# Optimization experiments

Measured on AMD Instinct MI355X. Metric: run time of the kernel, lower is better.

## Reference

```python
import jax, jax.numpy as jnp
import numpy as np

B, T = 64, 64
H = 256
CLIP = 0.2


def _conv(x, W, b, s):
    y = jax.lax.conv_general_dilated(x, W, (s, s), 'VALID',
                                     dimension_numbers=('NHWC', 'HWIO', 'NHWC'))
    return jax.nn.leaky_relu(y + b, negative_slope=0.2)


def _lstm(x, Wk, Wr, b):
    # keras LSTM, gate order i,f,g,o; x: (B,T,256) -> (B,T,256)
    h0 = jnp.zeros((x.shape[0], H), x.dtype)

    def step(carry, xt):
        h, c = carry
        z = xt @ Wk + h @ Wr + b
        i, f, g, o = jnp.split(z, 4, axis=-1)
        c = jax.nn.sigmoid(f) * c + jax.nn.sigmoid(i) * jnp.tanh(g)
        h = jax.nn.sigmoid(o) * jnp.tanh(c)
        return (h, c), h

    _, hs = jax.lax.scan(step, (h0, h0), jnp.swapaxes(x, 0, 1))
    return jnp.swapaxes(hs, 0, 1)


def setup_inputs():
    key = jax.random.key(0)
    ks = jax.random.split(key, 24)
    s = 0.05
    x = jax.random.normal(ks[0], (B, T, 13, 8, 8), jnp.float32)
    a_taken = jax.random.randint(ks[1], (B, T), 0, 36)
    mask = jax.random.randint(ks[2], (B, T, 4096), 0, 2).astype(jnp.int32)
    # taken actions must be legal (mask=1), as in real rollouts
    bi = jnp.repeat(jnp.arange(B), T)
    ti = jnp.tile(jnp.arange(T), B)
    mask = mask.at[bi, ti, a_taken.reshape(-1)].set(1)
    lg_prob_old = -jnp.abs(jax.random.normal(ks[3], (B, T), jnp.float32)) - 1.0
    GAE = jax.random.normal(ks[4], (B, T), jnp.float32)
    old_v_pred = jax.random.normal(ks[5], (B, T), jnp.float32)
    returns = jax.random.normal(ks[6], (B, T), jnp.float32)
    return {
        'x': x, 'mask': mask, 'lg_prob_old': lg_prob_old, 'a_taken': a_taken,
        'GAE': GAE, 'old_v_pred': old_v_pred, 'returns': returns,
        'W1': jax.random.normal(ks[7], (2, 2, 8, 16), jnp.float32) * s,
        'b1': jnp.zeros((16,), jnp.float32),
        'W2': jax.random.normal(ks[8], (2, 2, 16, 32), jnp.float32) * s,
        'b2': jnp.zeros((32,), jnp.float32),
        'W3': jax.random.normal(ks[9], (2, 2, 32, 64), jnp.float32) * s,
        'b3': jnp.zeros((64,), jnp.float32),
        'W4': jax.random.normal(ks[10], (1, 1, 64, 128), jnp.float32) * s,
        'b4': jnp.zeros((128,), jnp.float32),
        'lstm_k': jax.random.normal(ks[11], (256, 1024), jnp.float32) * s,
        'lstm_r': jax.random.normal(ks[12], (256, 1024), jnp.float32) * s,
        'lstm_b': jnp.zeros((1024,), jnp.float32),
        'pir_W': jax.random.normal(ks[13], (256, 36), jnp.float32) * s,
        'pir_b': jnp.zeros((36,), jnp.float32),
        'pim_W': jax.random.normal(ks[14], (256, 4096), jnp.float32) * s,
        'pim_b': jnp.zeros((4096,), jnp.float32),
        'v_W': jax.random.normal(ks[15], (256, 1), jnp.float32) * s,
        'v_b': jnp.zeros((1,), jnp.float32),
    }


def reference(x, mask, lg_prob_old, a_taken, GAE, old_v_pred, returns,
              W1, b1, W2, b2, W3, b3, W4, b4,
              lstm_k, lstm_r, lstm_b, pir_W, pir_b, pim_W, pim_b, v_W, v_b):
    Bn, Tn = x.shape[0], x.shape[1]
    h = x.reshape(Bn * Tn, 13, 8, 8)  # NHWC: H=13, W=8, C=8
    h = _conv(h, W1, b1, 2)  # (BT,6,4,16)
    h = _conv(h, W2, b2, 1)  # (BT,5,3,32)
    h = _conv(h, W3, b3, 2)  # (BT,2,1,64)
    h = _conv(h, W4, b4, 1)  # (BT,2,1,128)
    # keras Flatten(data_format='channels_first') permutes dim1 to last then flattens
    h = jnp.transpose(h, (0, 2, 3, 1)).reshape(Bn, Tn, -1)  # (B,T,256)
    lstm = _lstm(h, lstm_k, lstm_r, lstm_b).reshape(-1, H)  # (BT,256)

    pir = jax.nn.softmax(lstm @ pir_W + pir_b, axis=-1)  # (BT,36)
    maskf = mask.reshape(-1, 4096).astype(jnp.float32)
    pim = jax.nn.softmax(lstm @ pim_W + pim_b, axis=-1) * maskf
    scale = jnp.sum(pim, axis=1, keepdims=True)
    pim = pim / jnp.where(scale > 0, scale, jnp.ones_like(scale))  # (BT,4096)
    vpred = lstm @ v_W + v_b  # (BT,1)

    lg_old = lg_prob_old.reshape(-1)
    a = a_taken.reshape(-1)
    gae = GAE.reshape(-1)
    ovp = old_v_pred.reshape(-1)
    ret = returns.reshape(-1)
    gae = (gae - jnp.mean(gae)) / (jnp.std(gae) + 1e-8)

    t = jnp.arange(a.shape[0])
    p = jnp.where(t % 2 == 0, pir[t, a], pim[t, a])  # alternating heads
    lg_new = jnp.log(p)
    rt = jnp.exp(lg_new - lg_old)
    pg1 = -gae * rt
    pg2 = -gae * jnp.clip(rt, 1.0 - CLIP, 1.0 + CLIP)
    pg_loss = jnp.mean(jnp.maximum(pg1, pg2))

    # faithful to original TF: (BT,1) vpred broadcast against (BT,) -> (BT,BT)
    vpredclipped = ovp + jnp.clip(vpred - ovp, -CLIP, CLIP)
    vf1 = jnp.square(vpred - ret)
    vf2 = jnp.square(vpredclipped - ret)
    vf_loss = 0.5 * jnp.mean(jnp.maximum(vf1, vf2))

    pim_e = pim + (1.0 - maskf)
    entropy = -jnp.sum(pir * jnp.log(pir)) - jnp.sum(pim_e * jnp.log(pim_e))
    loss = pg_loss - entropy + vf_loss
    return (loss, pg_loss, entropy, vf_loss)
```

## Files before the change

kernel.cpp:

```cpp
#include <hip/hip_runtime.h>

typedef unsigned short u16;
typedef unsigned int   u32;

#define BT   4096
#define TSEQ 64
#define NB   64

typedef __attribute__((ext_vector_type(8))) short  short8;
typedef __attribute__((ext_vector_type(4))) float  f32x4;
typedef __attribute__((ext_vector_type(2))) _Float16 h2;

__device__ __forceinline__ float bf(u16 v) {
    u32 u = ((u32)v) << 16;
    return __builtin_bit_cast(float, u);
}
__device__ __forceinline__ u16 f2b(float f) {
    u32 u = __builtin_bit_cast(u32, f);
    return (u16)((u + 0x7fffu + ((u >> 16) & 1u)) >> 16);
}
__device__ __forceinline__ float lrelu(float x) { return x > 0.f ? x : 0.2f * x; }
__device__ __forceinline__ h2 i2h(int v) { return __builtin_bit_cast(h2, v); }
__device__ __forceinline__ float dot2(int hbits, int wbits, float acc) {
#if __has_builtin(__builtin_amdgcn_fdot2)
    return __builtin_amdgcn_fdot2(i2h(hbits), i2h(wbits), acc, false);
#else
    h2 a = i2h(hbits), b = i2h(wbits);
    return acc + (float)a.x * (float)b.x + (float)a.y * (float)b.y;
#endif
}
__device__ __forceinline__ float fsigm(float x) { return 1.f / (1.f + __expf(-x)); }
__device__ __forceinline__ float ftanh(float x) { return 1.f - 2.f / (__expf(2.f * x) + 1.f); }
__device__ __forceinline__ float ldf(const void* p, int i, int f32) {
    return f32 ? ((const float*)p)[i] : bf(((const u16*)p)[i]);
}
__device__ __forceinline__ u16 ldb(const void* p, int i, int f32) {
    return f32 ? f2b(((const float*)p)[i]) : ((const u16*)p)[i];
}

struct PrepPtrs {
    const void *x, *W1, *b1, *W2, *b2, *W3, *b3, *W4, *b4;
    const void *Wr, *Wk, *Wpim, *Wpir, *Wv;
    const u16* probe;
    u16 *featbf, *PF, *PBk, *PBpim, *PBpir;
    float* scal; int* flag;
};

#define PACK_BLKS 776
#define CONV_BLKS 2048

__global__ __launch_bounds__(256) void prep_kernel(PrepPtrs P)
{
    const int bid = blockIdx.x, tid = threadIdx.x;
    const int lane = tid & 63;
    u16 pv = P.probe[2 * lane];
    int e = (pv >> 7) & 0xFF;
    unsigned long long m = __ballot(pv == 0 || (e >= 100 && e <= 130));
    const int f32 = (__popcll(m) < 48) ? 1 : 0;

    if (bid == 0 && tid < 32) { P.scal[tid] = 0.f; if (tid == 0) *P.flag = f32; }

    if (bid < PACK_BLKS) {
        u16 t8[8];
        if (bid < 128) {
            int gid = bid * 256 + tid;
            int col = gid & 1023, oct = gid >> 10;
#pragma unroll
            for (int j = 0; j < 8; j++) {
                float f = ldf(P.Wr, (oct * 8 + j) * 1024 + col, f32);
                _Float16 h = (_Float16)f;
                t8[j] = __builtin_bit_cast(unsigned short, h);
            }
            *(int4*)&P.PF[((size_t)oct * 1024 + col) * 8] = *(int4*)t8;
        } else if (bid < 256) {
            int gid = (bid - 128) * 256 + tid;
            int col = gid & 1023, oct = gid >> 10;
#pragma unroll
            for (int j = 0; j < 8; j++) t8[j] = ldb(P.Wk, (oct * 8 + j) * 1024 + col, f32);
            *(int4*)&P.PBk[((((size_t)(oct >> 2) << 10) + col) * 4 + (oct & 3)) * 8] = *(int4*)t8;
        } else if (bid < 768) {
            int gid = (bid - 256) * 256 + tid;
            int col = gid & 4095, oct = gid >> 12;
#pragma unroll
            for (int j = 0; j < 8; j++) t8[j] = ldb(P.Wpim, (size_t)(oct * 8 + j) * 4096 + col, f32);
            *(int4*)&P.PBpim[((((size_t)(oct >> 2) << 12) + col) * 4 + (oct & 3)) * 8] = *(int4*)t8;
        } else {
            int gid = (bid - 768) * 256 + tid;
            int col = gid & 63, oct = gid >> 6;
#pragma unroll
            for (int j = 0; j < 8; j++) {
                int k = oct * 8 + j;
                u16 v = 0;
                if (col < 36)       v = ldb(P.Wpir, k * 36 + col, f32);
                else if (col == 36) v = ldb(P.Wv, k, f32);
                t8[j] = v;
            }
            *(int4*)&P.PBpir[(((size_t)(oct >> 2) * 64 + col) * 4 + (oct & 3)) * 8] = *(int4*)t8;
        }
        return;
    }

    __shared__ __align__(16) u16 wl[19184];
    __shared__ float xs[2][832];
    __shared__ float c1[2][384];
    __shared__ float c2[2][480];
    __shared__ float c3[2][128];
    const int pair = bid - PACK_BLKS;
    const int sub = tid >> 7, stid = tid & 127;
    const int bt = pair * 2 + sub;

    {
        const void* sp[8] = {P.W1, P.b1, P.W2, P.b2, P.W3, P.b3, P.W4, P.b4};
        const int   sn[8] = {512, 16, 2048, 32, 8192, 64, 8192, 128};
        int o = 0;
        for (int s = 0; s < 8; s++) {
            for (int i = tid; i < sn[s]; i += 256) wl[o + i] = ldb(sp[s], i, f32);
            o += sn[s];
        }
    }
    for (int i = stid; i < 832; i += 128) xs[sub][i] = ldf(P.x, bt * 832 + i, f32);
    __syncthreads();

    for (int idx = stid; idx < 96; idx += 128) {
        int pos = idx >> 2, g = idx & 3;
        int oh = pos >> 2, ow = pos & 3;
        float a0 = bf(wl[512 + g * 4]), a1 = bf(wl[513 + g * 4]),
              a2 = bf(wl[514 + g * 4]), a3 = bf(wl[515 + g * 4]);
        for (int kh = 0; kh < 2; kh++)
            for (int kw = 0; kw < 2; kw++)
#pragma unroll
                for (int ic = 0; ic < 8; ic++) {
                    float xv = xs[sub][(2 * oh + kh) * 64 + (2 * ow + kw) * 8 + ic];
                    ushort4 w = *(const ushort4*)&wl[((kh * 2 + kw) * 8 + ic) * 16 + g * 4];
                    a0 += xv * bf(w.x); a1 += xv * bf(w.y);
                    a2 += xv * bf(w.z); a3 += xv * bf(w.w);
                }
        c1[sub][pos * 16 + g * 4]     = lrelu(a0);
        c1[sub][pos * 16 + g * 4 + 1] = lrelu(a1);
        c1[sub][pos * 16 + g * 4 + 2] = lrelu(a2);
        c1[sub][pos * 16 + g * 4 + 3] = lrelu(a3);
    }
    __syncthreads();

    for (int idx = stid; idx < 120; idx += 128) {
        int pos = idx >> 3, g = idx & 7;
        int oh = pos / 3, ow = pos % 3;
        float a0 = bf(wl[2576 + g * 4]), a1 = bf(wl[2577 + g * 4]),
              a2 = bf(wl[2578 + g * 4]), a3 = bf(wl[2579 + g * 4]);
        for (int kh = 0; kh < 2; kh++)
            for (int kw = 0; kw < 2; kw++)
#pragma unroll
                for (int ic = 0; ic < 16; ic++) {
                    float xv = c1[sub][((oh + kh) * 4 + (ow + kw)) * 16 + ic];
                    ushort4 w = *(const ushort4*)&wl[528 + ((kh * 2 + kw) * 16 + ic) * 32 + g * 4];
                    a0 += xv * bf(w.x); a1 += xv * bf(w.y);
                    a2 += xv * bf(w.z); a3 += xv * bf(w.w);
                }
        c2[sub][pos * 32 + g * 4]     = lrelu(a0);
        c2[sub][pos * 32 + g * 4 + 1] = lrelu(a1);
        c2[sub][pos * 32 + g * 4 + 2] = lrelu(a2);
        c2[sub][pos * 32 + g * 4 + 3] = lrelu(a3);
    }
    __syncthreads();

    for (int idx = stid; idx < 32; idx += 128) {
        int oh = idx >> 4, g = idx & 15;
        float a0 = bf(wl[10800 + g * 4]), a1 = bf(wl[10801 + g * 4]),
              a2 = bf(wl[10802 + g * 4]), a3 = bf(wl[10803 + g * 4]);
        for (int kh = 0; kh < 2; kh++)
            for (int kw = 0; kw < 2; kw++)
#pragma unroll
                for (int ic = 0; ic < 32; ic++) {
                    float xv = c2[sub][((2 * oh + kh) * 3 + kw) * 32 + ic];
                    ushort4 w = *(const ushort4*)&wl[2608 + ((kh * 2 + kw) * 32 + ic) * 64 + g * 4];
                    a0 += xv * bf(w.x); a1 += xv * bf(w.y);
                    a2 += xv * bf(w.z); a3 += xv * bf(w.w);
                }
        c3[sub][oh * 64 + g * 4]     = lrelu(a0);
        c3[sub][oh * 64 + g * 4 + 1] = lrelu(a1);
        c3[sub][oh * 64 + g * 4 + 2] = lrelu(a2);
        c3[sub][oh * 64 + g * 4 + 3] = lrelu(a3);
    }
    __syncthreads();

    for (int idx = stid; idx < 64; idx += 128) {
        int oh = idx >> 5, g = idx & 31;
        float a0 = bf(wl[19056 + g * 4]), a1 = bf(wl[19057 + g * 4]),
              a2 = bf(wl[19058 + g * 4]), a3 = bf(wl[19059 + g * 4]);
#pragma unroll
        for (int ic = 0; ic < 64; ic++) {
            float xv = c3[sub][oh * 64 + ic];
            ushort4 w = *(const ushort4*)&wl[10864 + ic * 128 + g * 4];
            a0 += xv * bf(w.x); a1 += xv * bf(w.y);
            a2 += xv * bf(w.z); a3 += xv * bf(w.w);
        }
        P.featbf[bt * 256 + (g * 4 + 0) * 2 + oh] = f2b(lrelu(a0));
        P.featbf[bt * 256 + (g * 4 + 1) * 2 + oh] = f2b(lrelu(a1));
        P.featbf[bt * 256 + (g * 4 + 2) * 2 + oh] = f2b(lrelu(a2));
        P.featbf[bt * 256 + (g * 4 + 3) * 2 + oh] = f2b(lrelu(a3));
    }
}

__global__ __launch_bounds__(256) void gemm_zx(
    const u16* __restrict__ Abf, const u16* __restrict__ PB,
    const void* __restrict__ bias, const int* __restrict__ flag,
    float* __restrict__ out)
{
    __shared__ __align__(16) u16 As[16 * 264];
    const int mb = blockIdx.y, nb = blockIdx.x, tid = threadIdx.x;
    const int f32 = *flag;
    const int m0 = mb * 16;
    {
        int row = tid >> 4, part = tid & 15;
        const f32x4* src = (const f32x4*)&Abf[(size_t)(m0 + row) * 256 + part * 16];
        f32x4 v0 = src[0], v1 = src[1];
        *(f32x4*)&As[row * 264 + part * 16] = v0;
        *(f32x4*)&As[row * 264 + part * 16 + 8] = v1;
    }
    __syncthreads();
    const int wv = tid >> 6, lane = tid & 63;
    const int colw = lane & 15, q = lane >> 4;
    const int n = nb * 64 + wv * 16 + colw;
    f32x4 acc = {0.f, 0.f, 0.f, 0.f};
#pragma unroll
    for (int kt = 0; kt < 8; kt++) {
        short8 a = *(const short8*)&As[colw * 264 + kt * 32 + q * 8];
        short8 b = *(const short8*)&PB[((((size_t)kt << 10) + n) * 4 + q) * 8];
        acc = __builtin_amdgcn_mfma_f32_16x16x32_bf16(a, b, acc, 0, 0, 0);
    }
    const float bj = ldf(bias, n, f32);
#pragma unroll
    for (int r = 0; r < 4; r++) {
        int row = q * 4 + r;
        out[(size_t)(m0 + row) * 1024 + n] = acc[r] + bj;
    }
}

#define NPRE 18
#define NLDS 7
#define NSTR (32 - NPRE - NLDS)
__global__ __launch_bounds__(1024)
__attribute__((amdgpu_waves_per_eu(4, 4)))
void lstm_kernel(
    const float* __restrict__ zx, const u16* __restrict__ PF,
    u16* __restrict__ hseqbf)
{
    __shared__ float zp[1024];
    __shared__ __align__(16) u16 h16[256];
    __shared__ u16 hist[TSEQ * 256];
    __shared__ __align__(16) int4 wlds[NLDS * 1024];
    const int b = blockIdx.x, tid = threadIdx.x;
    float c = 0.f;
    const int4* Pw = (const int4*)PF;

    int4 wr[NPRE];
#pragma unroll
    for (int j = 0; j < NPRE; j++) wr[j] = Pw[j * 1024 + tid];
#pragma unroll
    for (int j = 0; j < NLDS; j++) wlds[j * 1024 + tid] = Pw[(NPRE + j) * 1024 + tid];
    if (tid < 256) h16[tid] = 0;
    __syncthreads();

    for (int t = 0; t < TSEQ; t++) {
        int4 ws[NSTR];
#pragma unroll
        for (int j = 0; j < NSTR; j++) ws[j] = Pw[(NPRE + NLDS + j) * 1024 + tid];
        float zxv = zx[(size_t)(b * TSEQ + t) * 1024 + tid];

        float a0 = 0.f, a1 = 0.f, a2 = 0.f, a3 = 0.f;
#pragma unroll
        for (int j = 0; j < NPRE; j++) {
            int4 hv = *(const int4*)&h16[j * 8];
            a0 = dot2(hv.x, wr[j].x, a0);
            a1 = dot2(hv.y, wr[j].y, a1);
            a2 = dot2(hv.z, wr[j].z, a2);
            a3 = dot2(hv.w, wr[j].w, a3);
        }
#pragma unroll
        for (int j = 0; j < NLDS; j++) {
            int4 hv = *(const int4*)&h16[(NPRE + j) * 8];
            int4 w = wlds[j * 1024 + tid];
            a0 = dot2(hv.x, w.x, a0);
            a1 = dot2(hv.y, w.y, a1);
            a2 = dot2(hv.z, w.z, a2);
            a3 = dot2(hv.w, w.w, a3);
        }
#pragma unroll
        for (int j = 0; j < NSTR; j++) {
            int4 hv = *(const int4*)&h16[(NPRE + NLDS + j) * 8];
            a0 = dot2(hv.x, ws[j].x, a0);
            a1 = dot2(hv.y, ws[j].y, a1);
            a2 = dot2(hv.z, ws[j].z, a2);
            a3 = dot2(hv.w, ws[j].w, a3);
        }
        zp[tid] = ((a0 + a1) + (a2 + a3)) + zxv;
        __syncthreads();
        if (tid < 256) {
            float ai = zp[tid], af = zp[256 + tid], ag = zp[512 + tid], ao = zp[768 + tid];
            float ig = fsigm(ai), fg = fsigm(af), og = fsigm(ao);
            float gg = ftanh(ag);
            c = fg * c + ig * gg;
            float h = og * ftanh(c);
            h16[tid] = __builtin_bit_cast(unsigned short, (_Float16)h);
            hist[t * 256 + tid] = f2b(h);
        }
        __syncthreads();
    }
    for (int i = tid; i < TSEQ * 256; i += 1024)
        hseqbf[(size_t)b * (TSEQ * 256) + i] = hist[i];
}

__global__ __launch_bounds__(256) void pir_kernel(
    const u16* __restrict__ Abf, const u16* __restrict__ PB,
    const void* __restrict__ pir_b, const void* __restrict__ v_b,
    const int* __restrict__ flag, const int* __restrict__ a_taken,
    float* __restrict__ entpir, float* __restrict__ ppira, float* __restrict__ vpred)
{
    __shared__ __align__(16) u16 As[64 * 264];
    const int tid = threadIdx.x;
    const int wv = tid >> 6, lane = tid & 63;
    const int colw = lane & 15, q = lane >> 4;
    const int f32 = *flag;
    const int m0 = blockIdx.x * 64;

    for (int idx = tid; idx < 1024; idx += 256) {
        int row = idx >> 4, part = idx & 15;
        const f32x4* src = (const f32x4*)&Abf[(size_t)(m0 + row) * 256 + part * 16];
        f32x4 v0 = src[0], v1 = src[1];
        *(f32x4*)&As[row * 264 + part * 16] = v0;
        *(f32x4*)&As[row * 264 + part * 16 + 8] = v1;
    }
    __syncthreads();
    f32x4 acc[4];
#pragma unroll
    for (int nt = 0; nt < 4; nt++) acc[nt] = (f32x4){0.f, 0.f, 0.f, 0.f};
#pragma unroll
    for (int kt = 0; kt < 8; kt++) {
        short8 a = *(const short8*)&As[(wv * 16 + colw) * 264 + kt * 32 + q * 8];
#pragma unroll
        for (int nt = 0; nt < 4; nt++) {
            short8 b = *(const short8*)&PB[((((size_t)kt * 64) + nt * 16 + colw) * 4 + q) * 8];
            acc[nt] = __builtin_amdgcn_mfma_f32_16x16x32_bf16(a, b, acc[nt], 0, 0, 0);
        }
    }
    float* zq = (float*)&As[wv * 4224];
#pragma unroll
    for (int nt = 0; nt < 4; nt++) {
        int col = nt * 16 + colw;
        float bj = (col < 36) ? ldf(pir_b, col, f32)
                              : (col == 36 ? ldf(v_b, 0, f32) : 0.f);
#pragma unroll
        for (int r = 0; r < 4; r++)
            zq[(q * 4 + r) * 65 + col] = acc[nt][r] + bj;
    }
    if (lane < 16) {
        int R = m0 + wv * 16 + lane;
        const float* zrow = &zq[lane * 65];
        float Z = 0.f, U = 0.f;
        for (int cc = 0; cc < 36; cc++) {
            float z = zrow[cc];
            float ev = __expf(z);
            Z += ev; U += ev * z;
        }
        entpir[R] = logf(Z) - U / Z;
        ppira[R]  = __expf(zrow[a_taken[R]]) / Z;
        vpred[R]  = zrow[36];
    }
}

__global__ __launch_bounds__(256) void pim_kernel(
    const u16* __restrict__ Abf, const u16* __restrict__ PB,
    const void* __restrict__ pim_b, const int* __restrict__ flag,
    const int* __restrict__ mask, const int* __restrict__ a_taken,
    float* __restrict__ partS, float* __restrict__ partU, float* __restrict__ za)
{
    __shared__ __align__(16) u16 As[32 * 264];
    __shared__ float redS[4][32], redU[4][32];
    const int nb = blockIdx.x, mb = blockIdx.y, tid = threadIdx.x;
    const int wv = tid >> 6, lane = tid & 63;
    const int colw = lane & 15, q = lane >> 4;
    const int f32 = *flag;
    const int m0 = mb * 32;

    for (int idx = tid; idx < 512; idx += 256) {
        int row = idx >> 4, part = idx & 15;
        const f32x4* src = (const f32x4*)&Abf[(size_t)(m0 + row) * 256 + part * 16];
        f32x4 v0 = src[0], v1 = src[1];
        *(f32x4*)&As[row * 264 + part * 16] = v0;
        *(f32x4*)&As[row * 264 + part * 16 + 8] = v1;
    }
    __syncthreads();
    const int n = nb * 64 + wv * 16 + colw;
    f32x4 acc0 = {0.f, 0.f, 0.f, 0.f}, acc1 = {0.f, 0.f, 0.f, 0.f};
#pragma unroll
    for (int kt = 0; kt < 8; kt++) {
        short8 b = *(const short8*)&PB[((((size_t)kt << 12) + n) * 4 + q) * 8];
        short8 a0 = *(const short8*)&As[colw * 264 + kt * 32 + q * 8];
        short8 a1 = *(const short8*)&As[(16 + colw) * 264 + kt * 32 + q * 8];
        acc0 = __builtin_amdgcn_mfma_f32_16x16x32_bf16(a0, b, acc0, 0, 0, 0);
        acc1 = __builtin_amdgcn_mfma_f32_16x16x32_bf16(a1, b, acc1, 0, 0, 0);
    }
    const float bj = ldf(pim_b, n, f32);
#pragma unroll
    for (int half = 0; half < 2; half++) {
        const f32x4& acc = half ? acc1 : acc0;
        float sv[4], uv[4];
#pragma unroll
        for (int r = 0; r < 4; r++) {
            int row = m0 + half * 16 + q * 4 + r;
            float z = acc[r] + bj;
            int mm = mask[(size_t)row * 4096 + n];
            float ev = __expf(z);
            sv[r] = mm ? ev : 0.f;
            uv[r] = mm ? ev * z : 0.f;
            if (n == a_taken[row]) za[row] = z;
        }
#pragma unroll
        for (int r = 0; r < 4; r++) {
            for (int off = 1; off < 16; off <<= 1) {
                sv[r] += __shfl_xor(sv[r], off, 16);
                uv[r] += __shfl_xor(uv[r], off, 16);
            }
            if (colw == 0) {
                redS[wv][half * 16 + q * 4 + r] = sv[r];
                redU[wv][half * 16 + q * 4 + r] = uv[r];
            }
        }
    }
    __syncthreads();
    if (tid < 32) {
        float S = redS[0][tid] + redS[1][tid] + redS[2][tid] + redS[3][tid];
        float U = redU[0][tid] + redU[1][tid] + redU[2][tid] + redU[3][tid];
        partS[(size_t)(m0 + tid) * 64 + nb] = S;
        partU[(size_t)(m0 + tid) * 64 + nb] = U;
    }
}

#define TAIL_BLOCKS (16 + 256)
__global__ __launch_bounds__(256) void tail_kernel(
    const float* __restrict__ partS, const float* __restrict__ partU,
    const float* __restrict__ za,
    const float* __restrict__ entpir, const float* __restrict__ ppira,
    const float* __restrict__ vpred,
    const void* __restrict__ lgold, const void* __restrict__ gae,
    const void* __restrict__ ovp, const void* __restrict__ ret,
    float* __restrict__ scal, const int* __restrict__ flag,
    void* __restrict__ out)
{
    const int bid = blockIdx.x, tid = threadIdx.x;
    const int f32 = *flag;
    __shared__ float sh[8];
    __shared__ float mst[2];
    if (bid < 16) {
        const int r = bid * 256 + tid;
        float S = 0.f, U = 0.f;
#pragma unroll
        for (int t2 = 0; t2 < 64; t2++) {
            S += partS[(size_t)r * 64 + t2];
            U += partU[(size_t)r * 64 + t2];
        }
        float entpim = logf(S) - U / S;
        float ppima = __expf(za[r]) / S;
        float s = 0.f, s2 = 0.f;
        if (f32) {
            const float* gp = (const float*)gae;
            for (int i = tid; i < BT; i += 256) { float v = gp[i]; s += v; s2 += v * v; }
        } else {
            const u16* gp = (const u16*)gae;
            for (int i = tid; i < BT; i += 256) { float v = bf(gp[i]); s += v; s2 += v * v; }
        }
        for (int off = 32; off; off >>= 1) {
            s += __shfl_down(s, off, 64); s2 += __shfl_down(s2, off, 64);
        }
        if ((tid & 63) == 0) { sh[tid >> 6] = s; sh[4 + (tid >> 6)] = s2; }
        __syncthreads();
        if (tid == 0) {
            float Sa = sh[0] + sh[1] + sh[2] + sh[3];
            float S2a = sh[4] + sh[5] + sh[6] + sh[7];
            float mean = Sa / (float)BT;
            float var = S2a / (float)BT - mean * mean;
            mst[0] = mean; mst[1] = sqrtf(fmaxf(var, 0.f));
        }
        __syncthreads();
        float mean = mst[0], sd = mst[1];
        float p = (r & 1) ? ppima : ppira[r];
        float ln = logf(p);
        float rt = __expf(ln - ldf(lgold, r, f32));
        float g = (ldf(gae, r, f32) - mean) / (sd + 1e-8f);
        float rtc = fminf(fmaxf(rt, 0.8f), 1.2f);
        float pg = fmaxf(-g * rt, -g * rtc);
        float e12 = entpir[r] + entpim;
        for (int off = 32; off; off >>= 1) {
            pg += __shfl_down(pg, off, 64);
            e12 += __shfl_down(e12, off, 64);
        }
        if ((tid & 63) == 0) {
            atomicAdd(&scal[2], pg);
            atomicAdd(&scal[3], e12);
        }
    } else {
        const int i0 = (bid - 16) * 16;
        float s = 0.f;
        if (f32) {
            const float* rp = (const float*)ret;
            const float* op = (const float*)ovp;
            for (int rr = 0; rr < 16; rr++) {
                float vp = vpred[i0 + rr];
                for (int j = tid; j < BT; j += 256) {
                    float r2 = rp[j], o = op[j];
                    float d = fminf(fmaxf(vp - o, -0.2f), 0.2f);
                    float v1 = vp - r2;    v1 *= v1;
                    float v2 = o + d - r2; v2 *= v2;
                    s += fmaxf(v1, v2);
                }
            }
        } else {
            const u16* rp = (const u16*)ret;
            const u16* op = (const u16*)ovp;
            for (int rr = 0; rr < 16; rr++) {
                float vp = vpred[i0 + rr];
                for (int j = tid; j < BT; j += 256) {
                    float r2 = bf(rp[j]), o = bf(op[j]);
                    float d = fminf(fmaxf(vp - o, -0.2f), 0.2f);
                    float v1 = vp - r2;    v1 *= v1;
                    float v2 = o + d - r2; v2 *= v2;
                    s += fmaxf(v1, v2);
                }
            }
        }
        for (int off = 32; off; off >>= 1) s += __shfl_down(s, off, 64);
        if ((tid & 63) == 0) sh[tid >> 6] = s;
        __syncthreads();
        if (tid == 0) atomicAdd(&scal[5], sh[0] + sh[1] + sh[2] + sh[3]);
    }
    __threadfence();
    __syncthreads();
    if (tid == 0) {
        unsigned old = atomicAdd((unsigned int*)&scal[8], 1u);
        if (old == TAIL_BLOCKS - 1) {
            __threadfence();
            float pgs = atomicAdd(&scal[2], 0.f);
            float ents = atomicAdd(&scal[3], 0.f);
            float vfs = atomicAdd(&scal[5], 0.f);
            float pg = pgs / (float)BT;
            float vf = 0.5f * vfs / ((float)BT * (float)BT);
            float loss = pg - ents + vf;
            if (f32) {
                float* o = (float*)out;
                o[0] = loss; o[1] = pg; o[2] = ents; o[3] = vf;
            } else {
                u16* o = (u16*)out;
                o[0] = f2b(loss); o[1] = f2b(pg); o[2] = f2b(ents); o[3] = f2b(vf);
            }
        }
    }
}

extern "C" void kernel_launch(void* const* d_in, const int* in_sizes, int n_in,
                              void* d_out, int out_size, void* d_ws, size_t ws_size,
                              hipStream_t stream)
{
    const int* mask = (const int*)d_in[1];
    const int* a_tk = (const int*)d_in[3];

    float* p = (float*)d_ws;
    u16*   featbf = (u16*)p;            p += 524288;
    float* zx     = p;                  p += 4194304;
    u16*   hseqbf = (u16*)p;            p += 524288;
    u16*   PF     = (u16*)p;            p += 131072;
    u16*   PBk    = (u16*)p;            p += 131072;
    u16*   PBpim  = (u16*)p;            p += 524288;
    u16*   PBpir  = (u16*)p;            p += 8192;
    float* scal   = p;                  p += 32;
    int*   flag   = (int*)p;            p += 4;
    float* partS  = p;                  p += 262144;
    float* partU  = p;                  p += 262144;
    float* za     = p;                  p += 4096;
    float* entpir = p;                  p += 4096;
    float* ppira  = p;                  p += 4096;
    float* vpred  = p;                  p += 4096;

    PrepPtrs P;
    P.x = d_in[0];
    P.W1 = d_in[7];  P.b1 = d_in[8];
    P.W2 = d_in[9];  P.b2 = d_in[10];
    P.W3 = d_in[11]; P.b3 = d_in[12];
    P.W4 = d_in[13]; P.b4 = d_in[14];
    P.Wk = d_in[15]; P.Wr = d_in[16];
    P.Wpir = d_in[18]; P.Wpim = d_in[20]; P.Wv = d_in[22];
    P.probe = (const u16*)d_in[15];
    P.featbf = featbf; P.PF = PF; P.PBk = PBk; P.PBpim = PBpim; P.PBpir = PBpir;
    P.scal = scal; P.flag = flag;

    prep_kernel<<<PACK_BLKS + CONV_BLKS, 256, 0, stream>>>(P);
    gemm_zx<<<dim3(16, 256), 256, 0, stream>>>(featbf, PBk, d_in[17], flag, zx);
    lstm_kernel<<<NB, 1024, 0, stream>>>(zx, PF, hseqbf);
    pir_kernel<<<64, 256, 0, stream>>>(hseqbf, PBpir, d_in[19], d_in[23], flag,
                                       a_tk, entpir, ppira, vpred);
    pim_kernel<<<dim3(64, 128), 256, 0, stream>>>(hseqbf, PBpim, d_in[21], flag,
                                                  mask, a_tk, partS, partU, za);
    tail_kernel<<<TAIL_BLOCKS, 256, 0, stream>>>(
        partS, partU, za, entpir, ppira, vpred,
        d_in[2], d_in[4], d_in[5], d_in[6], scal, flag, (void*)d_out);
}
```

Before: 488.8 us.

## Store LSTM recurrent weights as fp8 e5m2 and merge head kernels

```diff
diff --git a/kernel.cpp b/kernel.cpp
--- a/kernel.cpp
+++ b/kernel.cpp
@@ -2,6 +2,7 @@
 
 typedef unsigned short u16;
 typedef unsigned int   u32;
+typedef unsigned char  u8;
 
 #define BT   4096
 #define TSEQ 64
@@ -29,6 +30,20 @@
     return acc + (float)a.x * (float)b.x + (float)a.y * (float)b.y;
 #endif
 }
+__device__ __forceinline__ int e5lo(int w) {
+#if __has_builtin(__builtin_amdgcn_perm)
+    return (int)__builtin_amdgcn_perm(0u, (u32)w, 0x010C000Cu);
+#else
+    return ((w & 0xFF) << 8) | ((w & 0xFF00) << 16);
+#endif
+}
+__device__ __forceinline__ int e5hi(int w) {
+#if __has_builtin(__builtin_amdgcn_perm)
+    return (int)__builtin_amdgcn_perm(0u, (u32)w, 0x030C020Cu);
+#else
+    return (((w >> 16) & 0xFF) << 8) | (w & 0xFF000000);
+#endif
+}
 __device__ __forceinline__ float fsigm(float x) { return 1.f / (1.f + __expf(-x)); }
 __device__ __forceinline__ float ftanh(float x) { return 1.f - 2.f / (__expf(2.f * x) + 1.f); }
 __device__ __forceinline__ float ldf(const void* p, int i, int f32) {
@@ -42,7 +57,8 @@
     const void *x, *W1, *b1, *W2, *b2, *W3, *b3, *W4, *b4;
     const void *Wr, *Wk, *Wpim, *Wpir, *Wv;
     const u16* probe;
-    u16 *featbf, *PF, *PBk, *PBpim, *PBpir;
+    u16 *featbf, *PBk, *PBpim, *PBpir;
+    u8* PF8;
     float* scal; int* flag;
 };
 
@@ -61,32 +77,35 @@
     if (bid == 0 && tid < 32) { P.scal[tid] = 0.f; if (tid == 0) *P.flag = f32; }
 
     if (bid < PACK_BLKS) {
-        u16 t8[8];
         if (bid < 128) {
             int gid = bid * 256 + tid;
             int col = gid & 1023, oct = gid >> 10;
+            u8 t8[8];
 #pragma unroll
             for (int j = 0; j < 8; j++) {
                 float f = ldf(P.Wr, (oct * 8 + j) * 1024 + col, f32);
-                _Float16 h = (_Float16)f;
-                t8[j] = __builtin_bit_cast(unsigned short, h);
-            }
-            *(int4*)&P.PF[((size_t)oct * 1024 + col) * 8] = *(int4*)t8;
+                u16 hb = __builtin_bit_cast(unsigned short, (_Float16)f);
+                t8[j] = (u8)((hb + 0x7Fu + ((hb >> 8) & 1u)) >> 8);
+            }
+            *(int2*)&P.PF8[((size_t)oct * 1024 + col) * 8] = *(int2*)t8;
         } else if (bid < 256) {
             int gid = (bid - 128) * 256 + tid;
             int col = gid & 1023, oct = gid >> 10;
+            u16 t8[8];
 #pragma unroll
             for (int j = 0; j < 8; j++) t8[j] = ldb(P.Wk, (oct * 8 + j) * 1024 + col, f32);
             *(int4*)&P.PBk[((((size_t)(oct >> 2) << 10) + col) * 4 + (oct & 3)) * 8] = *(int4*)t8;
         } else if (bid < 768) {
             int gid = (bid - 256) * 256 + tid;
             int col = gid & 4095, oct = gid >> 12;
+            u16 t8[8];
 #pragma unroll
             for (int j = 0; j < 8; j++) t8[j] = ldb(P.Wpim, (size_t)(oct * 8 + j) * 4096 + col, f32);
             *(int4*)&P.PBpim[((((size_t)(oct >> 2) << 12) + col) * 4 + (oct & 3)) * 8] = *(int4*)t8;
         } else {
             int gid = (bid - 768) * 256 + tid;
             int col = gid & 63, oct = gid >> 6;
+            u16 t8[8];
 #pragma unroll
             for (int j = 0; j < 8; j++) {
                 int k = oct * 8 + j;
@@ -236,62 +255,50 @@
     }
 }
 
-#define NPRE 18
-#define NLDS 7
-#define NSTR (32 - NPRE - NLDS)
+#define NLDS8 8
+#define NSTR8 (32 - NLDS8)
 __global__ __launch_bounds__(1024)
 __attribute__((amdgpu_waves_per_eu(4, 4)))
 void lstm_kernel(
-    const float* __restrict__ zx, const u16* __restrict__ PF,
+    const float* __restrict__ zx, const u8* __restrict__ PF8,
     u16* __restrict__ hseqbf)
 {
     __shared__ float zp[1024];
     __shared__ __align__(16) u16 h16[256];
     __shared__ u16 hist[TSEQ * 256];
-    __shared__ __align__(16) int4 wlds[NLDS * 1024];
+    __shared__ __align__(8) int2 wlds[NLDS8 * 1024];
     const int b = blockIdx.x, tid = threadIdx.x;
     float c = 0.f;
-    const int4* Pw = (const int4*)PF;
-
-    int4 wr[NPRE];
-#pragma unroll
-    for (int j = 0; j < NPRE; j++) wr[j] = Pw[j * 1024 + tid];
-#pragma unroll
-    for (int j = 0; j < NLDS; j++) wlds[j * 1024 + tid] = Pw[(NPRE + j) * 1024 + tid];
+    const int2* Pw = (const int2*)PF8;
+
+#pragma unroll
+    for (int j = 0; j < NLDS8; j++) wlds[j * 1024 + tid] = Pw[j * 1024 + tid];
     if (tid < 256) h16[tid] = 0;
     __syncthreads();
 
     for (int t = 0; t < TSEQ; t++) {
-        int4 ws[NSTR];
-#pragma unroll
-        for (int j = 0; j < NSTR; j++) ws[j] = Pw[(NPRE + NLDS + j) * 1024 + tid];
+        int2 ws[NSTR8];
+#pragma unroll
+        for (int j = 0; j < NSTR8; j++) ws[j] = Pw[(NLDS8 + j) * 1024 + tid];
         float zxv = zx[(size_t)(b * TSEQ + t) * 1024 + tid];
 
         float a0 = 0.f, a1 = 0.f, a2 = 0.f, a3 = 0.f;
 #pragma unroll
-        for (int j = 0; j < NPRE; j++) {
+        for (int j = 0; j < NLDS8; j++) {
             int4 hv = *(const int4*)&h16[j * 8];
-            a0 = dot2(hv.x, wr[j].x, a0);
-            a1 = dot2(hv.y, wr[j].y, a1);
-            a2 = dot2(hv.z, wr[j].z, a2);
-            a3 = dot2(hv.w, wr[j].w, a3);
-        }
-#pragma unroll
-        for (int j = 0; j < NLDS; j++) {
-            int4 hv = *(const int4*)&h16[(NPRE + j) * 8];
-            int4 w = wlds[j * 1024 + tid];
-            a0 = dot2(hv.x, w.x, a0);
-            a1 = dot2(hv.y, w.y, a1);
-            a2 = dot2(hv.z, w.z, a2);
-            a3 = dot2(hv.w, w.w, a3);
-        }
-#pragma unroll
-        for (int j = 0; j < NSTR; j++) {
-            int4 hv = *(const int4*)&h16[(NPRE + NLDS + j) * 8];
-            a0 = dot2(hv.x, ws[j].x, a0);
-            a1 = dot2(hv.y, ws[j].y, a1);
-            a2 = dot2(hv.z, ws[j].z, a2);
-            a3 = dot2(hv.w, ws[j].w, a3);
+            int2 w = wlds[j * 1024 + tid];
+            a0 = dot2(hv.x, e5lo(w.x), a0);
+            a1 = dot2(hv.y, e5hi(w.x), a1);
+            a2 = dot2(hv.z, e5lo(w.y), a2);
+            a3 = dot2(hv.w, e5hi(w.y), a3);
+        }
+#pragma unroll
+        for (int j = 0; j < NSTR8; j++) {
+            int4 hv = *(const int4*)&h16[(NLDS8 + j) * 8];
+            a0 = dot2(hv.x, e5lo(ws[j].x), a0);
+            a1 = dot2(hv.y, e5hi(ws[j].x), a1);
+            a2 = dot2(hv.z, e5lo(ws[j].y), a2);
+            a3 = dot2(hv.w, e5hi(ws[j].y), a3);
         }
         zp[tid] = ((a0 + a1) + (a2 + a3)) + zxv;
         __syncthreads();
@@ -310,78 +317,71 @@
         hseqbf[(size_t)b * (TSEQ * 256) + i] = hist[i];
 }
 
-__global__ __launch_bounds__(256) void pir_kernel(
-    const u16* __restrict__ Abf, const u16* __restrict__ PB,
-    const void* __restrict__ pir_b, const void* __restrict__ v_b,
-    const int* __restrict__ flag, const int* __restrict__ a_taken,
-    float* __restrict__ entpir, float* __restrict__ ppira, float* __restrict__ vpred)
+__global__ __launch_bounds__(256) void heads_kernel(
+    const u16* __restrict__ Abf,
+    const u16* __restrict__ PBpim, const u16* __restrict__ PBpir,
+    const void* __restrict__ pim_b, const void* __restrict__ pir_b,
+    const void* __restrict__ v_b, const int* __restrict__ flag,
+    const int* __restrict__ mask, const int* __restrict__ a_taken,
+    float* __restrict__ entpir, float* __restrict__ ppira, float* __restrict__ vpred,
+    float* __restrict__ partS, float* __restrict__ partU, float* __restrict__ za)
 {
     __shared__ __align__(16) u16 As[64 * 264];
+    __shared__ float redS[4][32], redU[4][32];
     const int tid = threadIdx.x;
     const int wv = tid >> 6, lane = tid & 63;
     const int colw = lane & 15, q = lane >> 4;
     const int f32 = *flag;
-    const int m0 = blockIdx.x * 64;
-
-    for (int idx = tid; idx < 1024; idx += 256) {
-        int row = idx >> 4, part = idx & 15;
-        const f32x4* src = (const f32x4*)&Abf[(size_t)(m0 + row) * 256 + part * 16];
-        f32x4 v0 = src[0], v1 = src[1];
-        *(f32x4*)&As[row * 264 + part * 16] = v0;
-        *(f32x4*)&As[row * 264 + part * 16 + 8] = v1;
-    }
-    __syncthreads();
-    f32x4 acc[4];
-#pragma unroll
-    for (int nt = 0; nt < 4; nt++) acc[nt] = (f32x4){0.f, 0.f, 0.f, 0.f};
-#pragma unroll
-    for (int kt = 0; kt < 8; kt++) {
-        short8 a = *(const short8*)&As[(wv * 16 + colw) * 264 + kt * 32 + q * 8];
+
+    if (blockIdx.y == 128) {
+        const int m0 = blockIdx.x * 64;
+        for (int idx = tid; idx < 1024; idx += 256) {
+            int row = idx >> 4, part = idx & 15;
+            const f32x4* src = (const f32x4*)&Abf[(size_t)(m0 + row) * 256 + part * 16];
+            f32x4 v0 = src[0], v1 = src[1];
+            *(f32x4*)&As[row * 264 + part * 16] = v0;
+            *(f32x4*)&As[row * 264 + part * 16 + 8] = v1;
+        }
+        __syncthreads();
+        f32x4 acc[4];
+#pragma unroll
+        for (int nt = 0; nt < 4; nt++) acc[nt] = (f32x4){0.f, 0.f, 0.f, 0.f};
+#pragma unroll
+        for (int kt = 0; kt < 8; kt++) {
+            short8 a = *(const short8*)&As[(wv * 16 + colw) * 264 + kt * 32 + q * 8];
+#pragma unroll
+            for (int nt = 0; nt < 4; nt++) {
+                short8 b = *(const short8*)&PBpir[((((size_t)kt * 64) + nt * 16 + colw) * 4 + q) * 8];
+                acc[nt] = __builtin_amdgcn_mfma_f32_16x16x32_bf16(a, b, acc[nt], 0, 0, 0);
+            }
+        }
+        float* zq = (float*)&As[wv * 4224];
 #pragma unroll
         for (int nt = 0; nt < 4; nt++) {
-            short8 b = *(const short8*)&PB[((((size_t)kt * 64) + nt * 16 + colw) * 4 + q) * 8];
-            acc[nt] = __builtin_amdgcn_mfma_f32_16x16x32_bf16(a, b, acc[nt], 0, 0, 0);
-        }
-    }
-    float* zq = (float*)&As[wv * 4224];
-#pragma unroll
-    for (int nt = 0; nt < 4; nt++) {
-        int col = nt * 16 + colw;
-        float bj = (col < 36) ? ldf(pir_b, col, f32)
-                              : (col == 36 ? ldf(v_b, 0, f32) : 0.f);
-#pragma unroll
-        for (int r = 0; r < 4; r++)
-            zq[(q * 4 + r) * 65 + col] = acc[nt][r] + bj;
-    }
-    if (lane < 16) {
-        int R = m0 + wv * 16 + lane;
-        const float* zrow = &zq[lane * 65];
-        float Z = 0.f, U = 0.f;
-        for (int cc = 0; cc < 36; cc++) {
-            float z = zrow[cc];
-            float ev = __expf(z);
-            Z += ev; U += ev * z;
-        }
-        entpir[R] = logf(Z) - U / Z;
-        ppira[R]  = __expf(zrow[a_taken[R]]) / Z;
-        vpred[R]  = zrow[36];
-    }
-}
-
-__global__ __launch_bounds__(256) void pim_kernel(
-    const u16* __restrict__ Abf, const u16* __restrict__ PB,
-    const void* __restrict__ pim_b, const int* __restrict__ flag,
-    const int* __restrict__ mask, const int* __restrict__ a_taken,
-    float* __restrict__ partS, float* __restrict__ partU, float* __restrict__ za)
-{
-    __shared__ __align__(16) u16 As[32 * 264];
-    __shared__ float redS[4][32], redU[4][32];
-    const int nb = blockIdx.x, mb = blockIdx.y, tid = threadIdx.x;
-    const int wv = tid >> 6, lane = tid & 63;
-    const int colw = lane & 15, q = lane >> 4;
-    const int f32 = *flag;
+            int col = nt * 16 + colw;
+            float bj = (col < 36) ? ldf(pir_b, col, f32)
+                                  : (col == 36 ? ldf(v_b, 0, f32) : 0.f);
+#pragma unroll
+            for (int r = 0; r < 4; r++)
+                zq[(q * 4 + r) * 65 + col] = acc[nt][r] + bj;
+        }
+        if (lane < 16) {
+            int R = m0 + wv * 16 + lane;
+            const float* zrow = &zq[lane * 65];
+            float Z = 0.f, U = 0.f;
+            for (int cc = 0; cc < 36; cc++) {
+                float z = zrow[cc];
+                float ev = __expf(z);
+                Z += ev; U += ev * z;
+            }
+            entpir[R] = logf(Z) - U / Z;
+            ppira[R]  = __expf(zrow[a_taken[R]]) / Z;
+            vpred[R]  = zrow[36];
+        }
+        return;
+    }
+    const int nb = blockIdx.x, mb = blockIdx.y;
     const int m0 = mb * 32;
-
     for (int idx = tid; idx < 512; idx += 256) {
         int row = idx >> 4, part = idx & 15;
         const f32x4* src = (const f32x4*)&Abf[(size_t)(m0 + row) * 256 + part * 16];
@@ -394,7 +394,7 @@
     f32x4 acc0 = {0.f, 0.f, 0.f, 0.f}, acc1 = {0.f, 0.f, 0.f, 0.f};
 #pragma unroll
     for (int kt = 0; kt < 8; kt++) {
-        short8 b = *(const short8*)&PB[((((size_t)kt << 12) + n) * 4 + q) * 8];
+        short8 b = *(const short8*)&PBpim[((((size_t)kt << 12) + n) * 4 + q) * 8];
         short8 a0 = *(const short8*)&As[colw * 264 + kt * 32 + q * 8];
         short8 a1 = *(const short8*)&As[(16 + colw) * 264 + kt * 32 + q * 8];
         acc0 = __builtin_amdgcn_mfma_f32_16x16x32_bf16(a0, b, acc0, 0, 0, 0);
@@ -567,7 +567,7 @@
     u16*   featbf = (u16*)p;            p += 524288;
     float* zx     = p;                  p += 4194304;
     u16*   hseqbf = (u16*)p;            p += 524288;
-    u16*   PF     = (u16*)p;            p += 131072;
+    u8*    PF8    = (u8*)p;             p += 65536;
     u16*   PBk    = (u16*)p;            p += 131072;
     u16*   PBpim  = (u16*)p;            p += 524288;
     u16*   PBpir  = (u16*)p;            p += 8192;
@@ -589,16 +589,16 @@
     P.Wk = d_in[15]; P.Wr = d_in[16];
     P.Wpir = d_in[18]; P.Wpim = d_in[20]; P.Wv = d_in[22];
     P.probe = (const u16*)d_in[15];
-    P.featbf = featbf; P.PF = PF; P.PBk = PBk; P.PBpim = PBpim; P.PBpir = PBpir;
+    P.featbf = featbf; P.PBk = PBk; P.PBpim = PBpim; P.PBpir = PBpir;
+    P.PF8 = PF8;
     P.scal = scal; P.flag = flag;
 
     prep_kernel<<<PACK_BLKS + CONV_BLKS, 256, 0, stream>>>(P);
     gemm_zx<<<dim3(16, 256), 256, 0, stream>>>(featbf, PBk, d_in[17], flag, zx);
-    lstm_kernel<<<NB, 1024, 0, stream>>>(zx, PF, hseqbf);
-    pir_kernel<<<64, 256, 0, stream>>>(hseqbf, PBpir, d_in[19], d_in[23], flag,
-                                       a_tk, entpir, ppira, vpred);
-    pim_kernel<<<dim3(64, 128), 256, 0, stream>>>(hseqbf, PBpim, d_in[21], flag,
-                                                  mask, a_tk, partS, partU, za);
+    lstm_kernel<<<NB, 1024, 0, stream>>>(zx, PF8, hseqbf);
+    heads_kernel<<<dim3(64, 129), 256, 0, stream>>>(
+        hseqbf, PBpim, PBpir, d_in[21], d_in[19], d_in[23], flag, mask, a_tk,
+        entpir, ppira, vpred, partS, partU, za);
     tail_kernel<<<TAIL_BLOCKS, 256, 0, stream>>>(
         partS, partU, za, entpir, ppira, vpred,
         d_in[2], d_in[4], d_in[5], d_in[6], scal, flag, (void*)d_out);
```

New measurement: 512.8 us. +4.9%, slower.
